# Kernel optimization log

Hardware: AMD Instinct MI355X
Metric: run time of the kernel (lower is better)

## Reference

```python
import jax, jax.numpy as jnp
import numpy as np

B, S, DX, DM, H = 4, 2048, 1024, 1024, 16
DK = DM // H


def setup_inputs() -> dict:
    key = jax.random.key(0)
    ks = jax.random.split(key, 12)
    s = 0.02
    inp = {
        "q": jax.random.normal(ks[0], (B, S, DX), jnp.float32),
        "k": jax.random.normal(ks[1], (B, S, DX), jnp.float32),
        "v": jax.random.normal(ks[2], (B, S, DX), jnp.float32),
        "wq": jax.random.normal(ks[3], (DX, DM), jnp.float32) * s,
        "bq": jnp.zeros((DM,), jnp.float32),
        "wk": jax.random.normal(ks[4], (DX, DM), jnp.float32) * s,
        "bk": jnp.zeros((DM,), jnp.float32),
        "wv": jax.random.normal(ks[5], (DX, DM), jnp.float32) * s,
        "bv": jnp.zeros((DM,), jnp.float32),
        "wo": jax.random.normal(ks[6], (DM, DX), jnp.float32) * s,
        "bo": jnp.zeros((DX,), jnp.float32),
        # causal boolean mask [B, S_q, S_k]; True = attend
        "mask": jnp.broadcast_to(jnp.tril(jnp.ones((S, S), bool)), (B, S, S)),
    }
    return inp


def reference(q, k, v, wq, bq, wk, bk, wv, bv, wo, bo, mask):
    # Linear projections: [B,S,DX] @ [DX,DM] -> [B,S,DM]
    qh = (q @ wq + bq).reshape(B, S, H, DK).transpose(0, 2, 1, 3)  # [B,H,S,DK]
    kh = (k @ wk + bk).reshape(B, S, H, DK).transpose(0, 2, 1, 3)
    vh = (v @ wv + bv).reshape(B, S, H, DK).transpose(0, 2, 1, 3)

    scores = jnp.einsum("bhqd,bhkd->bhqk", qh, kh) / jnp.sqrt(jnp.float32(DK))
    neg = -jnp.finfo(scores.dtype).max
    scores = jnp.where(mask[:, None, :, :], scores, neg)  # mask.unsqueeze(1)
    p = jax.nn.softmax(scores, axis=-1)  # dropout inactive (eval / p=0)
    z = jnp.einsum("bhqk,bhkd->bhqd", p, vh)  # [B,H,S,DK]
    z = z.transpose(0, 2, 1, 3).reshape(B, S, DM)
    return z @ wo + bo
```

## Files before the change

### kernel.cpp

```cpp
#include <hip/hip_runtime.h>
#include <hip/hip_bf16.h>
#include <cstdint>

constexpr int Bb = 4, Sq = 2048, DXc = 1024, DMc = 1024, NH = 16, DKc = 64;
constexpr int GM = Bb * Sq;

typedef __attribute__((ext_vector_type(8))) short short8;
typedef __attribute__((ext_vector_type(4))) float f32x4;

__device__ inline unsigned short f2b(float f) {
  union { float f; uint32_t i; } c; c.f = f;
  uint32_t lsb = (c.i >> 16) & 1;
  c.i += 0x7fffu + lsb;
  return (unsigned short)(c.i >> 16);
}

__device__ inline uint32_t cvt_pk_bf16(float lo, float hi) {
  uint32_t r;
  asm("v_cvt_pk_bf16_f32 %0, %1, %2" : "=v"(r) : "v"(lo), "v"(hi));
  return r;
}

__device__ inline void load16_lds(const unsigned short* g, unsigned short* l) {
  __builtin_amdgcn_global_load_lds(
      (const __attribute__((address_space(1))) void*)g,
      (__attribute__((address_space(3))) void*)l, 16, 0, 0);
}

__global__ __launch_bounds__(256) void wt4_k(
    const float* __restrict__ wq, const float* __restrict__ wk,
    const float* __restrict__ wv, const float* __restrict__ wo,
    unsigned short* __restrict__ wqt, unsigned short* __restrict__ wkt,
    unsigned short* __restrict__ wvt, unsigned short* __restrict__ wot) {
  const int z = blockIdx.z;
  const float* W = z == 0 ? wq : z == 1 ? wk : z == 2 ? wv : wo;
  unsigned short* WT = z == 0 ? wqt : z == 1 ? wkt : z == 2 ? wvt : wot;
  __shared__ float t[64][65];
  const int tid = threadIdx.x;
  const int k0 = blockIdx.y * 64, n0 = blockIdx.x * 64;
#pragma unroll
  for (int p = 0; p < 4; ++p) {
    const int c = tid + p * 256;
    const int r = c >> 4, c4 = (c & 15) << 2;
    float4 v = *(const float4*)&W[(size_t)(k0 + r) * 1024 + n0 + c4];
    t[r][c4 + 0] = v.x; t[r][c4 + 1] = v.y; t[r][c4 + 2] = v.z; t[r][c4 + 3] = v.w;
  }
  __syncthreads();
#pragma unroll
  for (int p = 0; p < 4; ++p) {
    const int c = tid + p * 256;
    const int n = c >> 4, k4 = (c & 15) << 2;
    ushort4 o;
    o.x = f2b(t[k4 + 0][n]); o.y = f2b(t[k4 + 1][n]);
    o.z = f2b(t[k4 + 2][n]); o.w = f2b(t[k4 + 3][n]);
    *(ushort4*)&WT[(size_t)(n0 + n) * 1024 + k0 + k4] = o;
  }
}

__global__ __launch_bounds__(256) void qkv_k(
    const float* __restrict__ q, const float* __restrict__ k,
    const float* __restrict__ v,
    const unsigned short* __restrict__ wqt, const unsigned short* __restrict__ wkt,
    const unsigned short* __restrict__ wvt,
    const float* __restrict__ bq, const float* __restrict__ bk,
    const float* __restrict__ bv,
    unsigned short* __restrict__ qh, unsigned short* __restrict__ kh,
    unsigned short* __restrict__ vh) {
  constexpr int K = 1024;
  __shared__ __align__(16) unsigned short As[2][128 * 32];
  __shared__ __align__(16) unsigned short Bs[2][128 * 32];
  const int z = blockIdx.z;
  const float* A = z == 0 ? q : z == 1 ? k : v;
  const unsigned short* BT = z == 0 ? wqt : z == 1 ? wkt : wvt;
  const float* bias = z == 0 ? bq : z == 1 ? bk : bv;
  unsigned short* outB = z == 0 ? qh : z == 1 ? kh : vh;

  const int tid = threadIdx.x;
  const int lane = tid & 63;
  const int quad = lane >> 4, l16 = lane & 15;
  const int w = tid >> 6;
  const int wrow = (w >> 1) * 64, wcol = (w & 1) * 64;
  const int m0 = blockIdx.y * 128, n0 = blockIdx.x * 128;

  const int s0 = tid, s1 = tid + 256;
  const int ar0 = s0 >> 2, ac0 = (s0 & 3) * 8;
  const int ar1 = s1 >> 2, ac1 = (s1 & 3) * 8;
  const int br0 = s0 >> 2, bk0 = (s0 & 3) << 3;
  const int br1 = s1 >> 2, bk1 = (s1 & 3) << 3;

  f32x4 acc[4][4];
#pragma unroll
  for (int i = 0; i < 4; ++i)
#pragma unroll
    for (int j = 0; j < 4; ++j) acc[i][j] = (f32x4){0.f, 0.f, 0.f, 0.f};

  {
    const float4 a0 = *(const float4*)&A[(size_t)(m0 + ar0) * K + ac0];
    const float4 a1 = *(const float4*)&A[(size_t)(m0 + ar0) * K + ac0 + 4];
    const float4 a2 = *(const float4*)&A[(size_t)(m0 + ar1) * K + ac1];
    const float4 a3 = *(const float4*)&A[(size_t)(m0 + ar1) * K + ac1 + 4];
    load16_lds(&BT[(size_t)(n0 + br0) * K + bk0], &Bs[0][s0 * 8]);
    load16_lds(&BT[(size_t)(n0 + br1) * K + bk1], &Bs[0][s1 * 8]);
    uint4 p0, p1;
    p0.x = cvt_pk_bf16(a0.x, a0.y); p0.y = cvt_pk_bf16(a0.z, a0.w);
    p0.z = cvt_pk_bf16(a1.x, a1.y); p0.w = cvt_pk_bf16(a1.z, a1.w);
    p1.x = cvt_pk_bf16(a2.x, a2.y); p1.y = cvt_pk_bf16(a2.z, a2.w);
    p1.z = cvt_pk_bf16(a3.x, a3.y); p1.w = cvt_pk_bf16(a3.z, a3.w);
    *(uint4*)&As[0][s0 * 8] = p0;
    *(uint4*)&As[0][s1 * 8] = p1;
  }
  __syncthreads();

  for (int t = 0; t < 32; ++t) {
    const int cur = t & 1, nxt = cur ^ 1;
    float4 a0, a1, a2, a3;
    if (t < 31) {
      const int kn = (t + 1) * 32;
      a0 = *(const float4*)&A[(size_t)(m0 + ar0) * K + kn + ac0];
      a1 = *(const float4*)&A[(size_t)(m0 + ar0) * K + kn + ac0 + 4];
      a2 = *(const float4*)&A[(size_t)(m0 + ar1) * K + kn + ac1];
      a3 = *(const float4*)&A[(size_t)(m0 + ar1) * K + kn + ac1 + 4];
      load16_lds(&BT[(size_t)(n0 + br0) * K + kn + bk0], &Bs[nxt][s0 * 8]);
      load16_lds(&BT[(size_t)(n0 + br1) * K + kn + bk1], &Bs[nxt][s1 * 8]);
    }

    short8 af[4], bf[4];
#pragma unroll
    for (int i = 0; i < 4; ++i)
      af[i] = *(const short8*)&As[cur][(wrow + i * 16 + l16) * 32 + quad * 8];
#pragma unroll
    for (int j = 0; j < 4; ++j)
      bf[j] = *(const short8*)&Bs[cur][(wcol + j * 16 + l16) * 32 + quad * 8];
#pragma unroll
    for (int i = 0; i < 4; ++i)
#pragma unroll
      for (int j = 0; j < 4; ++j)
        acc[i][j] = __builtin_amdgcn_mfma_f32_16x16x32_bf16(af[i], bf[j], acc[i][j], 0, 0, 0);

    if (t < 31) {
      uint4 p0, p1;
      p0.x = cvt_pk_bf16(a0.x, a0.y); p0.y = cvt_pk_bf16(a0.z, a0.w);
      p0.z = cvt_pk_bf16(a1.x, a1.y); p0.w = cvt_pk_bf16(a1.z, a1.w);
      p1.x = cvt_pk_bf16(a2.x, a2.y); p1.y = cvt_pk_bf16(a2.z, a2.w);
      p1.z = cvt_pk_bf16(a3.x, a3.y); p1.w = cvt_pk_bf16(a3.z, a3.w);
      *(uint4*)&As[nxt][s0 * 8] = p0;
      *(uint4*)&As[nxt][s1 * 8] = p1;
    }
    __syncthreads();
  }

  float bvv[4];
#pragma unroll
  for (int j = 0; j < 4; ++j) bvv[j] = bias[n0 + wcol + j * 16 + l16];
#pragma unroll
  for (int i = 0; i < 4; ++i)
#pragma unroll
    for (int j = 0; j < 4; ++j)
#pragma unroll
      for (int r = 0; r < 4; ++r) {
        const int m = m0 + wrow + i * 16 + quad * 4 + r;
        const int n = n0 + wcol + j * 16 + l16;
        const float val = acc[i][j][r] + bvv[j];
        const int b = m >> 11, s = m & 2047, h = n >> 6, d = n & 63;
        if (z < 2) {
          outB[(((size_t)(b * NH + h) * Sq + s) << 6) + d] = f2b(val);
        } else {
          outB[(((size_t)(b * NH + h) * DKc + d) << 11) + s] = f2b(val);
        }
      }
}

__global__ __launch_bounds__(256) void mgemm_o(
    const unsigned short* __restrict__ A, const unsigned short* __restrict__ BT,
    const float* __restrict__ bias, float* __restrict__ outF) {
  constexpr int K = 1024;
  __shared__ __align__(16) unsigned short As[2][128 * 32];
  __shared__ __align__(16) unsigned short Bs[2][128 * 32];
  const int tid = threadIdx.x;
  const int lane = tid & 63;
  const int quad = lane >> 4, l16 = lane & 15;
  const int w = tid >> 6;
  const int wrow = (w >> 1) * 64, wcol = (w & 1) * 64;
  const int m0 = blockIdx.y * 128, n0 = blockIdx.x * 128;

  const int s0 = tid, s1 = tid + 256;
  const int r0 = s0 >> 2, c0 = (s0 & 3) << 3;
  const int r1 = s1 >> 2, c1 = (s1 & 3) << 3;

  f32x4 acc[4][4];
#pragma unroll
  for (int i = 0; i < 4; ++i)
#pragma unroll
    for (int j = 0; j < 4; ++j) acc[i][j] = (f32x4){0.f, 0.f, 0.f, 0.f};

  load16_lds(&A[(size_t)(m0 + r0) * K + c0], &As[0][s0 * 8]);
  load16_lds(&A[(size_t)(m0 + r1) * K + c1], &As[0][s1 * 8]);
  load16_lds(&BT[(size_t)(n0 + r0) * K + c0], &Bs[0][s0 * 8]);
  load16_lds(&BT[(size_t)(n0 + r1) * K + c1], &Bs[0][s1 * 8]);
  __syncthreads();

  for (int t = 0; t < 32; ++t) {
    const int cur = t & 1, nxt = cur ^ 1;
    if (t < 31) {
      const int kn = (t + 1) * 32;
      load16_lds(&A[(size_t)(m0 + r0) * K + kn + c0], &As[nxt][s0 * 8]);
      load16_lds(&A[(size_t)(m0 + r1) * K + kn + c1], &As[nxt][s1 * 8]);
      load16_lds(&BT[(size_t)(n0 + r0) * K + kn + c0], &Bs[nxt][s0 * 8]);
      load16_lds(&BT[(size_t)(n0 + r1) * K + kn + c1], &Bs[nxt][s1 * 8]);
    }

    short8 af[4], bf[4];
#pragma unroll
    for (int i = 0; i < 4; ++i)
      af[i] = *(const short8*)&As[cur][(wrow + i * 16 + l16) * 32 + quad * 8];
#pragma unroll
    for (int j = 0; j < 4; ++j)
      bf[j] = *(const short8*)&Bs[cur][(wcol + j * 16 + l16) * 32 + quad * 8];
#pragma unroll
    for (int i = 0; i < 4; ++i)
#pragma unroll
      for (int j = 0; j < 4; ++j)
        acc[i][j] = __builtin_amdgcn_mfma_f32_16x16x32_bf16(af[i], bf[j], acc[i][j], 0, 0, 0);

    __syncthreads();
  }

  float bv[4];
#pragma unroll
  for (int j = 0; j < 4; ++j) bv[j] = bias[n0 + wcol + j * 16 + l16];
#pragma unroll
  for (int i = 0; i < 4; ++i)
#pragma unroll
    for (int j = 0; j < 4; ++j)
#pragma unroll
      for (int r = 0; r < 4; ++r) {
        const int m = m0 + wrow + i * 16 + quad * 4 + r;
        const int n = n0 + wcol + j * 16 + l16;
        outF[(size_t)m * 1024 + n] = acc[i][j][r] + bv[j];
      }
}

__global__ __launch_bounds__(512) void flash_k(
    const unsigned short* __restrict__ Qh, const unsigned short* __restrict__ Kh,
    const unsigned short* __restrict__ Vt, unsigned short* __restrict__ Zb) {
  constexpr int LDP = 72;
  __shared__ __align__(16) unsigned short Klds[64 * 64];
  __shared__ __align__(16) unsigned short Vlds[64 * 64];
  __shared__ __align__(16) unsigned short Plds[8 * 16 * LDP];
  const int tid = threadIdx.x;
  const int w = tid >> 6, lane = tid & 63;
  const int quad = lane >> 4, l16 = lane & 15;
  const int bh = blockIdx.x & 63;
  const int qi = blockIdx.x >> 6;
  const int qa = qi * 128;
  const int qbv = (15 - qi) * 128;
  const size_t base = (size_t)bh * Sq * DKc;
  unsigned short* Pw = &Plds[w * 16 * LDP];

  const int qb[2] = {qa + w * 16, qbv + (7 - w) * 16};
  const int tiles_s[2] = {2 * qi + 1 + (w >= 4 ? 1 : 0),
                          31 - 2 * qi + (w < 4 ? 1 : 0)};
  const int ntile = 32 - 2 * qi;

  short8 qf0[2], qf1[2];
#pragma unroll
  for (int s = 0; s < 2; ++s) {
    const unsigned short* qp = Qh + base + (size_t)(qb[s] + l16) * DKc + quad * 8;
    qf0[s] = *(const short8*)qp;
    qf1[s] = *(const short8*)(qp + 32);
  }

  f32x4 oacc[2][4];
#pragma unroll
  for (int s = 0; s < 2; ++s)
#pragma unroll
    for (int n = 0; n < 4; ++n) oacc[s][n] = (f32x4){0.f, 0.f, 0.f, 0.f};
  float lsum[2] = {0.f, 0.f};

  const int row0 = tid >> 3, sp0 = tid & 7, gs0 = sp0 ^ (row0 & 7);
  const int pos0 = quad ^ (l16 & 7);
  const int pos1 = pos0 ^ 4;

  for (int it = 0; it < ntile; ++it) {
    const int kt0 = it * 64;
    __syncthreads();
    load16_lds(Kh + base + (size_t)(kt0 + row0) * DKc + gs0 * 8, &Klds[tid * 8]);
    load16_lds(Vt + base + (size_t)row0 * Sq + kt0 + gs0 * 8, &Vlds[tid * 8]);
    __syncthreads();

    short8 kf0[4], kf1[4];
#pragma unroll
    for (int t = 0; t < 4; ++t) {
      const int krow = (t * 16 + l16) * 64;
      kf0[t] = *(const short8*)&Klds[krow + pos0 * 8];
      kf1[t] = *(const short8*)&Klds[krow + pos1 * 8];
    }

#pragma unroll
    for (int s = 0; s < 2; ++s) {
      if (it >= tiles_s[s]) continue;
      f32x4 st[4];
#pragma unroll
      for (int t = 0; t < 4; ++t) {
        f32x4 z4 = (f32x4){0.f, 0.f, 0.f, 0.f};
        z4 = __builtin_amdgcn_mfma_f32_16x16x32_bf16(kf0[t], qf0[s], z4, 0, 0, 0);
        st[t] = __builtin_amdgcn_mfma_f32_16x16x32_bf16(kf1[t], qf1[s], z4, 0, 0, 0);
      }
      const int qrow = qb[s] + l16;
      float p[4][4];
      if (it == tiles_s[s] - 1) {
#pragma unroll
        for (int t = 0; t < 4; ++t)
#pragma unroll
          for (int r = 0; r < 4; ++r) {
            const int key = kt0 + t * 16 + quad * 4 + r;
            const float e = __expf(fminf(st[t][r] * 0.125f, 30.f));
            p[t][r] = (key <= qrow) ? e : 0.f;
          }
      } else {
#pragma unroll
        for (int t = 0; t < 4; ++t)
#pragma unroll
          for (int r = 0; r < 4; ++r)
            p[t][r] = __expf(fminf(st[t][r] * 0.125f, 30.f));
      }
#pragma unroll
      for (int t = 0; t < 4; ++t)
#pragma unroll
        for (int r = 0; r < 4; ++r) lsum[s] += p[t][r];
#pragma unroll
      for (int t = 0; t < 4; ++t) {
        ushort4 pk;
        pk.x = f2b(p[t][0]); pk.y = f2b(p[t][1]);
        pk.z = f2b(p[t][2]); pk.w = f2b(p[t][3]);
        *(ushort4*)&Pw[l16 * LDP + t * 16 + quad * 4] = pk;
      }
      short8 pf0 = *(const short8*)&Pw[l16 * LDP + quad * 8];
      short8 pf1 = *(const short8*)&Pw[l16 * LDP + 32 + quad * 8];
#pragma unroll
      for (int n = 0; n < 4; ++n) {
        const int vrow = (n * 16 + l16) * 64;
        short8 vf0 = *(const short8*)&Vlds[vrow + pos0 * 8];
        short8 vf1 = *(const short8*)&Vlds[vrow + pos1 * 8];
        oacc[s][n] = __builtin_amdgcn_mfma_f32_16x16x32_bf16(pf0, vf0, oacc[s][n], 0, 0, 0);
        oacc[s][n] = __builtin_amdgcn_mfma_f32_16x16x32_bf16(pf1, vf1, oacc[s][n], 0, 0, 0);
      }
    }
  }

  const int b = bh >> 4, h = bh & 15;
#pragma unroll
  for (int s = 0; s < 2; ++s) {
    float ls = lsum[s];
    ls += __shfl_xor(ls, 16, 64);
    ls += __shfl_xor(ls, 32, 64);
    const float inv = 1.f / ls;
    float invr[4];
#pragma unroll
    for (int r = 0; r < 4; ++r) invr[r] = __shfl(inv, quad * 4 + r, 64);
#pragma unroll
    for (int r = 0; r < 4; ++r) {
      const int row = qb[s] + quad * 4 + r;
      unsigned short* zp = Zb + ((size_t)b * Sq + row) * DMc + h * 64;
#pragma unroll
      for (int n = 0; n < 4; ++n) zp[n * 16 + l16] = f2b(oacc[s][n][r] * invr[r]);
    }
  }
}

extern "C" void kernel_launch(void* const* d_in, const int* in_sizes, int n_in,
                              void* d_out, int out_size, void* d_ws, size_t ws_size,
                              hipStream_t stream) {
  const float* q  = (const float*)d_in[0];
  const float* k  = (const float*)d_in[1];
  const float* v  = (const float*)d_in[2];
  const float* wq = (const float*)d_in[3];
  const float* bq = (const float*)d_in[4];
  const float* wk = (const float*)d_in[5];
  const float* bk = (const float*)d_in[6];
  const float* wv = (const float*)d_in[7];
  const float* bv = (const float*)d_in[8];
  const float* wo = (const float*)d_in[9];
  const float* bo = (const float*)d_in[10];

  constexpr size_t NEL = (size_t)GM * DMc;
  unsigned short* qh  = (unsigned short*)d_ws;
  unsigned short* kh  = qh + NEL;
  unsigned short* vh  = kh + NEL;
  unsigned short* xbf = vh + NEL;
  unsigned short* wqt = xbf + NEL;
  unsigned short* wkt = wqt + (size_t)DXc * DMc;
  unsigned short* wvt = wkt + (size_t)DXc * DMc;
  unsigned short* wot = wvt + (size_t)DXc * DMc;

  wt4_k<<<dim3(16, 16, 4), 256, 0, stream>>>(wq, wk, wv, wo, wqt, wkt, wvt, wot);
  qkv_k<<<dim3(8, 64, 3), 256, 0, stream>>>(q, k, v, wqt, wkt, wvt,
                                            bq, bk, bv, qh, kh, vh);
  flash_k<<<dim3(512), 512, 0, stream>>>(qh, kh, vh, xbf);
  mgemm_o<<<dim3(8, 64), 256, 0, stream>>>(xbf, wot, bo, (float*)d_out);
}
```

Measured before the change: 408.1 us.

## Triple-buffer GEMM LDS pipelines with vmcnt waits and remap QKV block order

```diff
diff --git a/kernel.cpp b/kernel.cpp
--- a/kernel.cpp
+++ b/kernel.cpp
@@ -67,9 +67,9 @@
     unsigned short* __restrict__ qh, unsigned short* __restrict__ kh,
     unsigned short* __restrict__ vh) {
   constexpr int K = 1024;
-  __shared__ __align__(16) unsigned short As[2][128 * 32];
-  __shared__ __align__(16) unsigned short Bs[2][128 * 32];
-  const int z = blockIdx.z;
+  __shared__ __align__(16) unsigned short As[3][128 * 32];
+  __shared__ __align__(16) unsigned short Bs[3][128 * 32];
+  const int z = blockIdx.y;
   const float* A = z == 0 ? q : z == 1 ? k : v;
   const unsigned short* BT = z == 0 ? wqt : z == 1 ? wkt : wvt;
   const float* bias = z == 0 ? bq : z == 1 ? bk : bv;
@@ -80,7 +80,9 @@
   const int quad = lane >> 4, l16 = lane & 15;
   const int w = tid >> 6;
   const int wrow = (w >> 1) * 64, wcol = (w & 1) * 64;
-  const int m0 = blockIdx.y * 128, n0 = blockIdx.x * 128;
+  int m0, n0;
+  { const int c = blockIdx.x & 7, kk = blockIdx.x >> 3;
+    n0 = (kk & 7) * 128; m0 = (c * 8 + (kk >> 3)) * 128; }
 
   const int s0 = tid, s1 = tid + 256;
   const int ar0 = s0 >> 2, ac0 = (s0 & 3) * 8;
@@ -94,59 +96,67 @@
 #pragma unroll
     for (int j = 0; j < 4; ++j) acc[i][j] = (f32x4){0.f, 0.f, 0.f, 0.f};
 
-  {
-    const float4 a0 = *(const float4*)&A[(size_t)(m0 + ar0) * K + ac0];
-    const float4 a1 = *(const float4*)&A[(size_t)(m0 + ar0) * K + ac0 + 4];
-    const float4 a2 = *(const float4*)&A[(size_t)(m0 + ar1) * K + ac1];
-    const float4 a3 = *(const float4*)&A[(size_t)(m0 + ar1) * K + ac1 + 4];
-    load16_lds(&BT[(size_t)(n0 + br0) * K + bk0], &Bs[0][s0 * 8]);
-    load16_lds(&BT[(size_t)(n0 + br1) * K + bk1], &Bs[0][s1 * 8]);
+#pragma unroll
+  for (int pt = 0; pt < 2; ++pt) {
+    const int kn = pt * 32;
+    const float4 a0 = *(const float4*)&A[(size_t)(m0 + ar0) * K + kn + ac0];
+    const float4 a1 = *(const float4*)&A[(size_t)(m0 + ar0) * K + kn + ac0 + 4];
+    const float4 a2 = *(const float4*)&A[(size_t)(m0 + ar1) * K + kn + ac1];
+    const float4 a3 = *(const float4*)&A[(size_t)(m0 + ar1) * K + kn + ac1 + 4];
+    load16_lds(&BT[(size_t)(n0 + br0) * K + kn + bk0], &Bs[pt][s0 * 8]);
+    load16_lds(&BT[(size_t)(n0 + br1) * K + kn + bk1], &Bs[pt][s1 * 8]);
     uint4 p0, p1;
     p0.x = cvt_pk_bf16(a0.x, a0.y); p0.y = cvt_pk_bf16(a0.z, a0.w);
     p0.z = cvt_pk_bf16(a1.x, a1.y); p0.w = cvt_pk_bf16(a1.z, a1.w);
     p1.x = cvt_pk_bf16(a2.x, a2.y); p1.y = cvt_pk_bf16(a2.z, a2.w);
     p1.z = cvt_pk_bf16(a3.x, a3.y); p1.w = cvt_pk_bf16(a3.z, a3.w);
-    *(uint4*)&As[0][s0 * 8] = p0;
-    *(uint4*)&As[0][s1 * 8] = p1;
-  }
-  __syncthreads();
+    *(uint4*)&As[pt][s0 * 8] = p0;
+    *(uint4*)&As[pt][s1 * 8] = p1;
+  }
+  asm volatile("s_waitcnt lgkmcnt(0)");
+  asm volatile("s_barrier" ::: "memory");
 
   for (int t = 0; t < 32; ++t) {
-    const int cur = t & 1, nxt = cur ^ 1;
+    const int c = t % 3;
     float4 a0, a1, a2, a3;
-    if (t < 31) {
-      const int kn = (t + 1) * 32;
+    if (t < 30) {
+      const int p = (t + 2) % 3;
+      const int kn = (t + 2) * 32;
       a0 = *(const float4*)&A[(size_t)(m0 + ar0) * K + kn + ac0];
       a1 = *(const float4*)&A[(size_t)(m0 + ar0) * K + kn + ac0 + 4];
       a2 = *(const float4*)&A[(size_t)(m0 + ar1) * K + kn + ac1];
       a3 = *(const float4*)&A[(size_t)(m0 + ar1) * K + kn + ac1 + 4];
-      load16_lds(&BT[(size_t)(n0 + br0) * K + kn + bk0], &Bs[nxt][s0 * 8]);
-      load16_lds(&BT[(size_t)(n0 + br1) * K + kn + bk1], &Bs[nxt][s1 * 8]);
+      load16_lds(&BT[(size_t)(n0 + br0) * K + kn + bk0], &Bs[p][s0 * 8]);
+      load16_lds(&BT[(size_t)(n0 + br1) * K + kn + bk1], &Bs[p][s1 * 8]);
     }
 
     short8 af[4], bf[4];
 #pragma unroll
     for (int i = 0; i < 4; ++i)
-      af[i] = *(const short8*)&As[cur][(wrow + i * 16 + l16) * 32 + quad * 8];
+      af[i] = *(const short8*)&As[c][(wrow + i * 16 + l16) * 32 + quad * 8];
 #pragma unroll
     for (int j = 0; j < 4; ++j)
-      bf[j] = *(const short8*)&Bs[cur][(wcol + j * 16 + l16) * 32 + quad * 8];
+      bf[j] = *(const short8*)&Bs[c][(wcol + j * 16 + l16) * 32 + quad * 8];
 #pragma unroll
     for (int i = 0; i < 4; ++i)
 #pragma unroll
       for (int j = 0; j < 4; ++j)
         acc[i][j] = __builtin_amdgcn_mfma_f32_16x16x32_bf16(af[i], bf[j], acc[i][j], 0, 0, 0);
 
-    if (t < 31) {
+    if (t < 30) {
+      const int p = (t + 2) % 3;
       uint4 p0, p1;
       p0.x = cvt_pk_bf16(a0.x, a0.y); p0.y = cvt_pk_bf16(a0.z, a0.w);
       p0.z = cvt_pk_bf16(a1.x, a1.y); p0.w = cvt_pk_bf16(a1.z, a1.w);
       p1.x = cvt_pk_bf16(a2.x, a2.y); p1.y = cvt_pk_bf16(a2.z, a2.w);
       p1.z = cvt_pk_bf16(a3.x, a3.y); p1.w = cvt_pk_bf16(a3.z, a3.w);
-      *(uint4*)&As[nxt][s0 * 8] = p0;
-      *(uint4*)&As[nxt][s1 * 8] = p1;
-    }
-    __syncthreads();
+      *(uint4*)&As[p][s0 * 8] = p0;
+      *(uint4*)&As[p][s1 * 8] = p1;
+      asm volatile("s_waitcnt vmcnt(2)");
+    } else {
+      asm volatile("s_waitcnt vmcnt(0)");
+    }
+    asm volatile("s_barrier" ::: "memory");
   }
 
   float bvv[4];
@@ -174,8 +184,8 @@
     const unsigned short* __restrict__ A, const unsigned short* __restrict__ BT,
     const float* __restrict__ bias, float* __restrict__ outF) {
   constexpr int K = 1024;
-  __shared__ __align__(16) unsigned short As[2][128 * 32];
-  __shared__ __align__(16) unsigned short Bs[2][128 * 32];
+  __shared__ __align__(16) unsigned short As[3][128 * 32];
+  __shared__ __align__(16) unsigned short Bs[3][128 * 32];
   const int tid = threadIdx.x;
   const int lane = tid & 63;
   const int quad = lane >> 4, l16 = lane & 15;
@@ -193,36 +203,47 @@
 #pragma unroll
     for (int j = 0; j < 4; ++j) acc[i][j] = (f32x4){0.f, 0.f, 0.f, 0.f};
 
-  load16_lds(&A[(size_t)(m0 + r0) * K + c0], &As[0][s0 * 8]);
-  load16_lds(&A[(size_t)(m0 + r1) * K + c1], &As[0][s1 * 8]);
-  load16_lds(&BT[(size_t)(n0 + r0) * K + c0], &Bs[0][s0 * 8]);
-  load16_lds(&BT[(size_t)(n0 + r1) * K + c1], &Bs[0][s1 * 8]);
-  __syncthreads();
+#pragma unroll
+  for (int pt = 0; pt < 2; ++pt) {
+    const int kn = pt * 32;
+    load16_lds(&A[(size_t)(m0 + r0) * K + kn + c0], &As[pt][s0 * 8]);
+    load16_lds(&A[(size_t)(m0 + r1) * K + kn + c1], &As[pt][s1 * 8]);
+    load16_lds(&BT[(size_t)(n0 + r0) * K + kn + c0], &Bs[pt][s0 * 8]);
+    load16_lds(&BT[(size_t)(n0 + r1) * K + kn + c1], &Bs[pt][s1 * 8]);
+  }
+  asm volatile("s_waitcnt vmcnt(4)");
+  asm volatile("s_barrier" ::: "memory");
 
   for (int t = 0; t < 32; ++t) {
-    const int cur = t & 1, nxt = cur ^ 1;
-    if (t < 31) {
-      const int kn = (t + 1) * 32;
-      load16_lds(&A[(size_t)(m0 + r0) * K + kn + c0], &As[nxt][s0 * 8]);
-      load16_lds(&A[(size_t)(m0 + r1) * K + kn + c1], &As[nxt][s1 * 8]);
-      load16_lds(&BT[(size_t)(n0 + r0) * K + kn + c0], &Bs[nxt][s0 * 8]);
-      load16_lds(&BT[(size_t)(n0 + r1) * K + kn + c1], &Bs[nxt][s1 * 8]);
+    const int cb = t % 3;
+    if (t < 30) {
+      const int p = (t + 2) % 3;
+      const int kn = (t + 2) * 32;
+      load16_lds(&A[(size_t)(m0 + r0) * K + kn + c0], &As[p][s0 * 8]);
+      load16_lds(&A[(size_t)(m0 + r1) * K + kn + c1], &As[p][s1 * 8]);
+      load16_lds(&BT[(size_t)(n0 + r0) * K + kn + c0], &Bs[p][s0 * 8]);
+      load16_lds(&BT[(size_t)(n0 + r1) * K + kn + c1], &Bs[p][s1 * 8]);
     }
 
     short8 af[4], bf[4];
 #pragma unroll
     for (int i = 0; i < 4; ++i)
-      af[i] = *(const short8*)&As[cur][(wrow + i * 16 + l16) * 32 + quad * 8];
+      af[i] = *(const short8*)&As[cb][(wrow + i * 16 + l16) * 32 + quad * 8];
 #pragma unroll
     for (int j = 0; j < 4; ++j)
-      bf[j] = *(const short8*)&Bs[cur][(wcol + j * 16 + l16) * 32 + quad * 8];
+      bf[j] = *(const short8*)&Bs[cb][(wcol + j * 16 + l16) * 32 + quad * 8];
 #pragma unroll
     for (int i = 0; i < 4; ++i)
 #pragma unroll
       for (int j = 0; j < 4; ++j)
         acc[i][j] = __builtin_amdgcn_mfma_f32_16x16x32_bf16(af[i], bf[j], acc[i][j], 0, 0, 0);
 
-    __syncthreads();
+    if (t < 30) {
+      asm volatile("s_waitcnt vmcnt(4)");
+    } else {
+      asm volatile("s_waitcnt vmcnt(0)");
+    }
+    asm volatile("s_barrier" ::: "memory");
   }
 
   float bv[4];
@@ -394,8 +415,8 @@
   unsigned short* wot = wvt + (size_t)DXc * DMc;
 
   wt4_k<<<dim3(16, 16, 4), 256, 0, stream>>>(wq, wk, wv, wo, wqt, wkt, wvt, wot);
-  qkv_k<<<dim3(8, 64, 3), 256, 0, stream>>>(q, k, v, wqt, wkt, wvt,
-                                            bq, bk, bv, qh, kh, vh);
+  qkv_k<<<dim3(512, 3), 256, 0, stream>>>(q, k, v, wqt, wkt, wvt,
+                                          bq, bk, bv, qh, kh, vh);
   flash_k<<<dim3(512), 512, 0, stream>>>(qh, kh, vh, xbf);
   mgemm_o<<<dim3(8, 64), 256, 0, stream>>>(xbf, wot, bo, (float*)d_out);
 }
```

Measured after the change: 406.5 us. No clear change (-0.4%).
